# Optimization experiments

Hardware: AMD Instinct MI355X
Metric: run time of the kernel (lower is better)

Reference implementation:

```python
import jax, jax.numpy as jnp
import numpy as np

DIM = 8      # channels (from CxWxW_Attention(8, 4, False))
HEADS = 4    # num_heads
EPS = 1e-12  # torch F.normalize eps


def setup_inputs() -> dict:
    key = jax.random.key(0)
    k0, k1, k2, k3 = jax.random.split(key, 4)
    b, c, h, w = 16, DIM, 512, 512
    x = jax.random.normal(k0, (b, c, h, w), jnp.float32)
    # 1x1 conv producing qkv (bias=False): weight (3c, c)
    w_qkv = jax.random.normal(k1, (3 * c, c), jnp.float32) * 0.1
    # 3x3 depthwise conv on qkv, groups=3c: weight (3c, 1, 3, 3)
    w_dw = jax.random.normal(k2, (3 * c, 1, 3, 3), jnp.float32) * 0.1
    # 1x1 projection out: weight (c, c)
    w_out = jax.random.normal(k3, (c, c), jnp.float32) * 0.1
    # per-head learned temperature, init ones; broadcasts over (b, head, c, w, w)
    temperature = jnp.ones((HEADS, 1, 1, 1), jnp.float32)
    return dict(x=x, w_qkv=w_qkv, w_dw=w_dw, w_out=w_out, temperature=temperature)


def _dwconv3x3(x, wgt):
    # depthwise 3x3, padding=1, groups = channels
    C = x.shape[1]
    return jax.lax.conv_general_dilated(
        x, wgt, window_strides=(1, 1), padding=((1, 1), (1, 1)),
        dimension_numbers=("NCHW", "OIHW", "NCHW"), feature_group_count=C)


def _l2norm(t):
    # torch.nn.functional.normalize along last dim
    n = jnp.sqrt(jnp.sum(t * t, axis=-1, keepdims=True))
    return t / jnp.maximum(n, EPS)


def reference(x, w_qkv, w_dw, w_out, temperature):
    b, c, h, w = x.shape
    heads, ch = HEADS, c // HEADS
    # qkv = dwconv3x3(conv1x1(x))
    qkv = jnp.einsum("bchw,oc->bohw", x, w_qkv)
    qkv = _dwconv3x3(qkv, w_dw)
    q, k, v = jnp.split(qkv, 3, axis=1)
    # rearrange 'b (head ch) h w -> b head ch w h' : width attends, height = feature
    def split_heads(t):
        return t.reshape(b, heads, ch, h, w).transpose(0, 1, 2, 4, 3)
    q, k, v = split_heads(q), split_heads(k), split_heads(v)
    q = _l2norm(q)
    k = _l2norm(k)
    # attention map of shape (b, head, ch, W, W)  -> the 'C x W x W' attention
    attn = jnp.einsum("bncwh,bncvh->bncwv", q, k) * temperature
    attn = jax.nn.softmax(attn, axis=-1)
    out = jnp.einsum("bncwv,bncvh->bncwh", attn, v)  # (b, head, ch, w, h)
    # rearrange back 'b head ch w h -> b (head ch) h w'
    out = out.transpose(0, 1, 2, 4, 3).reshape(b, c, h, w)
    return jnp.einsum("bchw,oc->bohw", out, w_out)
```

## Files before the change

### kernel.cpp

```cpp
#include <hip/hip_runtime.h>
#include <hip/hip_bf16.h>

typedef __attribute__((ext_vector_type(4))) float f32x4;
typedef __attribute__((ext_vector_type(2))) float f32x2;
typedef __attribute__((ext_vector_type(8))) short s16x8;
typedef __attribute__((ext_vector_type(4))) short s16x4;
typedef __attribute__((ext_vector_type(4))) unsigned short u16x4;

#define HW 512
#define NSLICE 128

__global__ __launch_bounds__(256) void qkv_fused(
    const float* __restrict__ x, const float* __restrict__ wqkv,
    const float* __restrict__ wdw,
    __hip_bfloat16* __restrict__ qT, __hip_bfloat16* __restrict__ kT,
    __hip_bfloat16* __restrict__ vS,
    float* __restrict__ qss, float* __restrict__ kss)
{
  const int b = blockIdx.y;
  const int tile = blockIdx.x;
  const int h0 = (tile >> 4) * 32;
  const int w0 = (tile & 15) * 32;
  const int tid = threadIdx.x;

  __shared__ float ts[4][1156][2];
  __shared__ __hip_bfloat16 ot[8][32][36];
  __shared__ float colsq[4][8][32];
  __shared__ float wq_s[24][8];
  __shared__ float wd_s[24][12];

  if (tid < 192) wq_s[tid >> 3][tid & 7] = wqkv[tid];
  if (tid < 216) wd_s[tid / 9][tid % 9] = wdw[tid];

  float xr[5][8];
  #pragma unroll
  for (int p = 0; p < 5; ++p) {
    int i = tid + p * 256;
    if (i < 1156) {
      int ih = h0 - 1 + i / 34, iw = w0 - 1 + i % 34;
      bool ok = (ih >= 0 && ih < HW && iw >= 0 && iw < HW);
      #pragma unroll
      for (int c = 0; c < 8; ++c) {
        xr[p][c] = ok ? x[((size_t)(b * 8 + c) * HW + ih) * HW + iw] : 0.f;
      }
    }
  }
  __syncthreads();

  const int tw = tid & 31;
  const int th = tid >> 5;
  const int lane = tid & 63;
  const int wv = tid >> 6;

  #pragma unroll
  for (int g = 0; g < 3; ++g) {
    #pragma unroll
    for (int p = 0; p < 5; ++p) {
      int i = tid + p * 256;
      if (i < 1156) {
        #pragma unroll
        for (int op = 0; op < 4; ++op) {
          const int o = g * 8 + op * 2;
          float a0 = 0.f, a1 = 0.f;
          #pragma unroll
          for (int c = 0; c < 8; ++c) {
            a0 += xr[p][c] * wq_s[o][c];
            a1 += xr[p][c] * wq_s[o + 1][c];
          }
          ts[op][i][0] = a0;
          ts[op][i][1] = a1;
        }
      }
    }
    __syncthreads();

    #pragma unroll
    for (int op = 0; op < 4; ++op) {
      const int o = g * 8 + op * 2;
      float w2[6][3][2];
      #pragma unroll
      for (int r = 0; r < 6; ++r)
        #pragma unroll
        for (int c = 0; c < 3; ++c) {
          f32x2 v = *(const f32x2*)&ts[op][(4 * th + r) * 34 + tw + c][0];
          w2[r][c][0] = v[0];
          w2[r][c][1] = v[1];
        }
      float o0[4], o1[4];
      #pragma unroll
      for (int r = 0; r < 4; ++r) { o0[r] = 0.f; o1[r] = 0.f; }
      #pragma unroll
      for (int di = 0; di < 3; ++di)
        #pragma unroll
        for (int dj = 0; dj < 3; ++dj) {
          const float wd0 = wd_s[o][di * 3 + dj];
          const float wd1 = wd_s[o + 1][di * 3 + dj];
          #pragma unroll
          for (int r = 0; r < 4; ++r) {
            o0[r] += w2[r + di][dj][0] * wd0;
            o1[r] += w2[r + di][dj][1] * wd1;
          }
        }
      if (g < 2) {
        float s0 = o0[0] * o0[0] + o0[1] * o0[1] + o0[2] * o0[2] + o0[3] * o0[3];
        float s1 = o1[0] * o1[0] + o1[1] * o1[1] + o1[2] * o1[2] + o1[3] * o1[3];
        s0 += __shfl_xor(s0, 32);
        s1 += __shfl_xor(s1, 32);
        if (lane < 32) {
          colsq[wv][op * 2][tw] = s0;
          colsq[wv][op * 2 + 1][tw] = s1;
        }
        #pragma unroll
        for (int r = 0; r < 4; ++r) {
          ot[op * 2][tw][4 * th + r] = __float2bfloat16(o0[r]);
          ot[op * 2 + 1][tw][4 * th + r] = __float2bfloat16(o1[r]);
        }
      } else {
        #pragma unroll
        for (int r = 0; r < 4; ++r) {
          ot[op * 2][4 * th + r][tw] = __float2bfloat16(o0[r]);
          ot[op * 2 + 1][4 * th + r][tw] = __float2bfloat16(o1[r]);
        }
      }
    }
    __syncthreads();

    {
      const int rr = tid >> 3, cc = tid & 7;
      #pragma unroll
      for (int o = 0; o < 8; ++o) {
        s16x4 v = *(const s16x4*)&ot[o][rr][cc * 4];
        const size_t sb = (size_t)(b * 8 + o) * HW * HW;
        if (g == 0) {
          *(s16x4*)(qT + sb + (size_t)(h0 >> 5) * HW * 32 + (size_t)(w0 + rr) * 32 + cc * 4) = v;
        } else if (g == 1) {
          *(s16x4*)(kT + sb + (size_t)(h0 >> 5) * HW * 32 + (size_t)(w0 + rr) * 32 + cc * 4) = v;
        } else {
          *(s16x4*)(vS + sb + (size_t)(w0 >> 5) * HW * 32 + (size_t)(h0 + rr) * 32 + cc * 4) = v;
        }
      }
    }
    if (g < 2) {
      const int o = tid >> 5, w = tid & 31;
      float s = colsq[0][o][w] + colsq[1][o][w] + colsq[2][o][w] + colsq[3][o][w];
      float* dst = (g == 0 ? qss : kss) + (size_t)(b * 8 + o) * HW + w0 + w;
      atomicAdd(dst, s);
    }
  }
}

#define LDS_P    0
#define OFF_RMAX 65536
#define OFF_RSUM 67584
#define OFF_RMAXF 69632
#define OFF_RSINV 69888
#define OFF_SQ   70144
#define OFF_SK   70400
#define ATTN_LDS_SIZE 72448

#define LOADQ(AF, S) { \
    const size_t cq_ = (size_t)(S) * 32768 + klo; \
    _Pragma("unroll") for (int m_ = 0; m_ < 4; ++m_) \
      AF[m_] = *(const s16x8*)(qs + cq_ + (size_t)(w0 + m_ * 16 + arow) * 64); }
#define LOADK(BF, S) { \
    const size_t ck_ = (size_t)(S) * 32768 + klo; \
    _Pragma("unroll") for (int n_ = 0; n_ < 4; ++n_) \
      BF[n_] = *(const s16x8*)(ks + ck_ + (size_t)(wv * 64 + n_ * 16 + arow) * 64); }
#define LOADV(BF, S) { \
    const size_t cv_ = (size_t)(S) * 32768 + klo; \
    _Pragma("unroll") for (int n_ = 0; n_ < 4; ++n_) \
      BF[n_] = *(const s16x8*)(vs + cv_ + (size_t)(wv * 64 + n_ * 16 + arow) * 64); }
#define LOADP(AF, S) { \
    const int cbp_ = (S) * 64 + klo; \
    _Pragma("unroll") for (int m_ = 0; m_ < 4; ++m_) { \
      const int row_ = m_ * 16 + arow; \
      AF[m_] = *(const s16x8*)(ldsP + row_ * 1024 + (cbp_ ^ ((row_ & 7) << 4))); } }
#define MFMA16(AF, BF, ACC) { \
    _Pragma("unroll") for (int m_ = 0; m_ < 4; ++m_) \
      _Pragma("unroll") for (int n_ = 0; n_ < 4; ++n_) \
        ACC[m_][n_] = __builtin_amdgcn_mfma_f32_16x16x32_bf16(AF[m_], BF[n_], ACC[m_][n_], 0, 0, 0); }

__global__ __launch_bounds__(512, 1) void attn_kernel(
    const __hip_bfloat16* __restrict__ qT, const __hip_bfloat16* __restrict__ kT,
    const __hip_bfloat16* __restrict__ vS, __hip_bfloat16* __restrict__ Obuf,
    const float* __restrict__ qss, const float* __restrict__ kss,
    const float* __restrict__ temp)
{
  extern __shared__ char smem[];
  char* ldsP = smem + LDS_P;
  float* red_max  = (float*)(smem + OFF_RMAX);
  float* red_sum  = (float*)(smem + OFF_RSUM);
  float* red_maxf = (float*)(smem + OFF_RMAXF);
  float* rsinv    = (float*)(smem + OFF_RSINV);
  float* sq_l     = (float*)(smem + OFF_SQ);
  float* sk_l     = (float*)(smem + OFF_SK);

  const int tid = threadIdx.x;
  const int lane = tid & 63;
  const int wv = tid >> 6;
  const int p = blockIdx.x;
  const int slice = (p & 7) + 8 * (p >> 6);
  const int rblk = (p >> 3) & 7;
  const int w0 = rblk * 64;
  const size_t sbase = (size_t)slice * HW * HW;
  const char* qs = (const char*)(qT + sbase);
  const char* ks = (const char*)(kT + sbase);
  const char* vs = (const char*)(vS + sbase);

  const int klo = (lane >> 4) << 4;
  const int arow = lane & 15;

  f32x4 acc[4][4];
  #pragma unroll
  for (int m = 0; m < 4; ++m)
    #pragma unroll
    for (int n = 0; n < 4; ++n) acc[m][n] = (f32x4){0.f, 0.f, 0.f, 0.f};

  const float tmp = temp[(slice & 7) >> 1];
  if (tid < 64) sq_l[tid] = tmp / fmaxf(sqrtf(qss[(size_t)slice * HW + w0 + tid]), 1e-12f);
  sk_l[tid] = 1.f / fmaxf(sqrtf(kss[(size_t)slice * HW + tid]), 1e-12f);

  for (int chn = 0; chn < 16; ++chn) {
    s16x8 af[4], bf[4];
    LOADQ(af, chn)
    LOADK(bf, chn)
    MFMA16(af, bf, acc)
  }
  __syncthreads();

  float srow[4][4], scol[4];
  #pragma unroll
  for (int m = 0; m < 4; ++m)
    #pragma unroll
    for (int r = 0; r < 4; ++r)
      srow[m][r] = sq_l[m * 16 + ((lane >> 4) << 2) + r];
  #pragma unroll
  for (int n = 0; n < 4; ++n) scol[n] = sk_l[wv * 64 + n * 16 + (lane & 15)];

  float rmax[4][4];
  #pragma unroll
  for (int m = 0; m < 4; ++m)
    #pragma unroll
    for (int r = 0; r < 4; ++r) {
      float mx = -1e30f;
      #pragma unroll
      for (int n = 0; n < 4; ++n) {
        float v = acc[m][n][r] * srow[m][r] * scol[n];
        acc[m][n][r] = v;
        mx = fmaxf(mx, v);
      }
      mx = fmaxf(mx, __shfl_xor(mx, 1));
      mx = fmaxf(mx, __shfl_xor(mx, 2));
      mx = fmaxf(mx, __shfl_xor(mx, 4));
      mx = fmaxf(mx, __shfl_xor(mx, 8));
      rmax[m][r] = mx;
    }
  if ((lane & 15) == 0) {
    #pragma unroll
    for (int m = 0; m < 4; ++m)
      #pragma unroll
      for (int r = 0; r < 4; ++r)
        red_max[(m * 16 + ((lane >> 4) << 2) + r) * 8 + wv] = rmax[m][r];
  }
  __syncthreads();
  if (tid < 64) {
    float mx = red_max[tid * 8];
    #pragma unroll
    for (int g = 1; g < 8; ++g) mx = fmaxf(mx, red_max[tid * 8 + g]);
    red_maxf[tid] = mx;
  }
  __syncthreads();

  float gmax[4][4];
  #pragma unroll
  for (int m = 0; m < 4; ++m)
    #pragma unroll
    for (int r = 0; r < 4; ++r)
      gmax[m][r] = red_maxf[m * 16 + ((lane >> 4) << 2) + r];

  float rs[4][4];
  #pragma unroll
  for (int m = 0; m < 4; ++m)
    #pragma unroll
    for (int r = 0; r < 4; ++r) rs[m][r] = 0.f;
  #pragma unroll
  for (int m = 0; m < 4; ++m)
    #pragma unroll
    for (int n = 0; n < 4; ++n)
      #pragma unroll
      for (int r = 0; r < 4; ++r) {
        int row = m * 16 + ((lane >> 4) << 2) + r;
        int col = wv * 64 + n * 16 + (lane & 15);
        float pv = __expf(acc[m][n][r] - gmax[m][r]);
        rs[m][r] += pv;
        *(__hip_bfloat16*)(ldsP + row * 1024 + ((col * 2) ^ ((row & 7) << 4))) =
            __float2bfloat16(pv);
      }
  #pragma unroll
  for (int m = 0; m < 4; ++m)
    #pragma unroll
    for (int r = 0; r < 4; ++r) {
      float s = rs[m][r];
      s += __shfl_xor(s, 1);
      s += __shfl_xor(s, 2);
      s += __shfl_xor(s, 4);
      s += __shfl_xor(s, 8);
      if ((lane & 15) == 0)
        red_sum[(m * 16 + ((lane >> 4) << 2) + r) * 8 + wv] = s;
    }
  __syncthreads();
  if (tid < 64) {
    float s = 0.f;
    #pragma unroll
    for (int g = 0; g < 8; ++g) s += red_sum[tid * 8 + g];
    rsinv[tid] = 1.f / s;
  }

  f32x4 acc2[4][4];
  #pragma unroll
  for (int m = 0; m < 4; ++m)
    #pragma unroll
    for (int n = 0; n < 4; ++n) acc2[m][n] = (f32x4){0.f, 0.f, 0.f, 0.f};

  for (int chn = 0; chn < 16; ++chn) {
    s16x8 af[4], bf[4];
    LOADP(af, chn)
    LOADV(bf, chn)
    MFMA16(af, bf, acc2)
  }
  __syncthreads();

  float rinv[4][4];
  #pragma unroll
  for (int m = 0; m < 4; ++m)
    #pragma unroll
    for (int r = 0; r < 4; ++r)
      rinv[m][r] = rsinv[m * 16 + ((lane >> 4) << 2) + r];

  char* ldsO = ldsP + wv * 8192;
  #pragma unroll
  for (int m = 0; m < 4; ++m)
    #pragma unroll
    for (int n = 0; n < 4; ++n)
      #pragma unroll
      for (int r = 0; r < 4; ++r) {
        int row = m * 16 + ((lane >> 4) << 2) + r;
        int col = n * 16 + (lane & 15);
        *(__hip_bfloat16*)(ldsO + row * 128 + col * 2) =
            __float2bfloat16(acc2[m][n][r] * rinv[m][r]);
      }
  __syncthreads();
  __hip_bfloat16* ob = Obuf + sbase + (size_t)w0 * HW + wv * 64;
  #pragma unroll
  for (int it = 0; it < 8; ++it) {
    int row = it * 8 + (lane >> 3);
    int c = (lane & 7) << 4;
    s16x8 v = *(const s16x8*)(ldsO + row * 128 + c);
    *(s16x8*)((char*)ob + (size_t)row * 1024 + c) = v;
  }
}

__global__ __launch_bounds__(256) void proj_kernel(
    const __hip_bfloat16* __restrict__ Obuf, const float* __restrict__ wout,
    float* __restrict__ out)
{
  const int b = blockIdx.y;
  const int t = blockIdx.x;
  const int h0 = (t >> 5) * 64;
  const int w0 = (t & 31) * 16;
  const int tid = threadIdx.x;
  __shared__ float os[8][16][65];
  __shared__ float wo_s[64];
  if (tid < 64) wo_s[tid] = wout[tid];
  {
    int r = tid >> 4;
    int c4 = (tid & 15) * 4;
    #pragma unroll
    for (int o = 0; o < 8; ++o) {
      const __hip_bfloat16* p = Obuf + ((size_t)(b * 8 + o) * HW + w0 + r) * HW + h0 + c4;
      u16x4 v = *(const u16x4*)p;
      #pragma unroll
      for (int i = 0; i < 4; ++i)
        os[o][r][c4 + i] = __uint_as_float((unsigned)v[i] << 16);
    }
  }
  __syncthreads();
  const int w = tid & 15;
  #pragma unroll
  for (int ih = 0; ih < 4; ++ih) {
    int h = ih * 16 + (tid >> 4);
    float ov[8];
    #pragma unroll
    for (int o = 0; o < 8; ++o) ov[o] = os[o][w][h];
    #pragma unroll
    for (int jo = 0; jo < 8; ++jo) {
      float a = 0.f;
      #pragma unroll
      for (int o = 0; o < 8; ++o) a += ov[o] * wo_s[jo * 8 + o];
      out[((size_t)(b * 8 + jo) * HW + h0 + h) * HW + w0 + w] = a;
    }
  }
}

extern "C" void kernel_launch(void* const* d_in, const int* in_sizes, int n_in,
                              void* d_out, int out_size, void* d_ws, size_t ws_size,
                              hipStream_t stream) {
  (void)in_sizes; (void)n_in; (void)out_size; (void)ws_size;
  const float* x    = (const float*)d_in[0];
  const float* wqkv = (const float*)d_in[1];
  const float* wdw  = (const float*)d_in[2];
  const float* wout = (const float*)d_in[3];
  const float* temp = (const float*)d_in[4];
  float* out = (float*)d_out;

  char* ws = (char*)d_ws;
  const size_t plane = (size_t)NSLICE * HW * HW * 2;
  __hip_bfloat16* qT = (__hip_bfloat16*)(ws);
  __hip_bfloat16* kT = (__hip_bfloat16*)(ws + plane);
  __hip_bfloat16* vS = (__hip_bfloat16*)(ws + 2 * plane);
  __hip_bfloat16* Ob = (__hip_bfloat16*)(ws + 3 * plane);
  float* qss = (float*)(ws + 4 * plane);
  float* kss = (float*)(ws + 4 * plane + (size_t)NSLICE * HW * 4);

  hipMemsetAsync(qss, 0, 2 * (size_t)NSLICE * HW * 4, stream);
  qkv_fused<<<dim3(256, 16), 256, 0, stream>>>(x, wqkv, wdw, qT, kT, vS, qss, kss);
  hipFuncSetAttribute((const void*)attn_kernel,
                      hipFuncAttributeMaxDynamicSharedMemorySize, ATTN_LDS_SIZE);
  attn_kernel<<<dim3(1024), 512, ATTN_LDS_SIZE, stream>>>(qT, kT, vS, Ob, qss, kss, temp);
  proj_kernel<<<dim3(256, 16), 256, 0, stream>>>(Ob, wout, out);
}
```

Before: 373.6 us.

## Software-pipeline QK and PV global loads with inline asm and manual vmcnt waits

Replaces the simple per-chunk load-then-MFMA loops in the attention kernel with a four-deep prefetch pipeline. It uses inline-asm global_load_dwordx4 and explicit s_waitcnt vmcnt counts. V tiles are prefetched before the softmax exponent phase so their latency overlaps with exp and LDS writes. This aims to hide global memory latency behind MFMA work, at the cost of many more live VGPRs and fragile hand-managed wait counts that bypass the compiler's scheduling.

```diff
diff --git a/kernel.cpp b/kernel.cpp
--- a/kernel.cpp
+++ b/kernel.cpp
@@ -158,18 +158,26 @@
 #define OFF_SK   70400
 #define ATTN_LDS_SIZE 72448
 
-#define LOADQ(AF, S) { \
-    const size_t cq_ = (size_t)(S) * 32768 + klo; \
-    _Pragma("unroll") for (int m_ = 0; m_ < 4; ++m_) \
-      AF[m_] = *(const s16x8*)(qs + cq_ + (size_t)(w0 + m_ * 16 + arow) * 64); }
-#define LOADK(BF, S) { \
-    const size_t ck_ = (size_t)(S) * 32768 + klo; \
-    _Pragma("unroll") for (int n_ = 0; n_ < 4; ++n_) \
-      BF[n_] = *(const s16x8*)(ks + ck_ + (size_t)(wv * 64 + n_ * 16 + arow) * 64); }
-#define LOADV(BF, S) { \
-    const size_t cv_ = (size_t)(S) * 32768 + klo; \
-    _Pragma("unroll") for (int n_ = 0; n_ < 4; ++n_) \
-      BF[n_] = *(const s16x8*)(vs + cv_ + (size_t)(wv * 64 + n_ * 16 + arow) * 64); }
+#define GL4(D, VOFF, BASE) \
+  asm volatile("global_load_dwordx4 %0, %1, %2 offset:0"    : "=v"(D[0]) : "v"(VOFF), "s"(BASE)); \
+  asm volatile("global_load_dwordx4 %0, %1, %2 offset:1024" : "=v"(D[1]) : "v"(VOFF), "s"(BASE)); \
+  asm volatile("global_load_dwordx4 %0, %1, %2 offset:2048" : "=v"(D[2]) : "v"(VOFF), "s"(BASE)); \
+  asm volatile("global_load_dwordx4 %0, %1, %2 offset:3072" : "=v"(D[3]) : "v"(VOFF), "s"(BASE));
+
+#define LOADSET1(AF, BF, CHN) { \
+  const char* bq_ = qs + (size_t)(CHN) * 32768; \
+  const char* bk_ = ks + (size_t)(CHN) * 32768; \
+  GL4(AF, voffQ, bq_) \
+  GL4(BF, voffK, bk_) }
+
+#define LOADSETV(VF, CHN) { \
+  const char* bv_ = vs + (size_t)(CHN) * 32768; \
+  GL4(VF, voffK, bv_) }
+
+#define WAITV(N) \
+  asm volatile("s_waitcnt vmcnt(" #N ")"); \
+  __builtin_amdgcn_sched_barrier(0);
+
 #define LOADP(AF, S) { \
     const int cbp_ = (S) * 64 + klo; \
     _Pragma("unroll") for (int m_ = 0; m_ < 4; ++m_) { \
@@ -209,6 +217,8 @@
 
   const int klo = (lane >> 4) << 4;
   const int arow = lane & 15;
+  const int voffQ = (w0 + arow) * 64 + klo;
+  const int voffK = (wv * 64 + arow) * 64 + klo;
 
   f32x4 acc[4][4];
   #pragma unroll
@@ -219,13 +229,25 @@
   const float tmp = temp[(slice & 7) >> 1];
   if (tid < 64) sq_l[tid] = tmp / fmaxf(sqrtf(qss[(size_t)slice * HW + w0 + tid]), 1e-12f);
   sk_l[tid] = 1.f / fmaxf(sqrtf(kss[(size_t)slice * HW + tid]), 1e-12f);
-
-  for (int chn = 0; chn < 16; ++chn) {
-    s16x8 af[4], bf[4];
-    LOADQ(af, chn)
-    LOADK(bf, chn)
-    MFMA16(af, bf, acc)
-  }
+  __builtin_amdgcn_sched_barrier(0);
+
+  s16x8 afA[4], bfA[4], afB[4], bfB[4], afC[4], bfC[4], afD[4], bfD[4];
+  LOADSET1(afA, bfA, 0)
+  LOADSET1(afB, bfB, 1)
+  LOADSET1(afC, bfC, 2)
+  LOADSET1(afD, bfD, 3)
+
+  #pragma unroll
+  for (int g = 0; g < 3; ++g) {
+    WAITV(24) MFMA16(afA, bfA, acc) LOADSET1(afA, bfA, 4 * g + 4)
+    WAITV(24) MFMA16(afB, bfB, acc) LOADSET1(afB, bfB, 4 * g + 5)
+    WAITV(24) MFMA16(afC, bfC, acc) LOADSET1(afC, bfC, 4 * g + 6)
+    WAITV(24) MFMA16(afD, bfD, acc) LOADSET1(afD, bfD, 4 * g + 7)
+  }
+  WAITV(24) MFMA16(afA, bfA, acc)
+  WAITV(16) MFMA16(afB, bfB, acc)
+  WAITV(8)  MFMA16(afC, bfC, acc)
+  WAITV(0)  MFMA16(afD, bfD, acc)
   __syncthreads();
 
   float srow[4][4], scol[4];
@@ -277,6 +299,12 @@
     #pragma unroll
     for (int r = 0; r < 4; ++r)
       gmax[m][r] = red_maxf[m * 16 + ((lane >> 4) << 2) + r];
+
+  s16x8 vfA[4], vfB[4], vfC[4], vfD[4];
+  LOADSETV(vfA, 0)
+  LOADSETV(vfB, 1)
+  LOADSETV(vfC, 2)
+  LOADSETV(vfD, 3)
 
   float rs[4][4];
   #pragma unroll
@@ -322,12 +350,17 @@
     #pragma unroll
     for (int n = 0; n < 4; ++n) acc2[m][n] = (f32x4){0.f, 0.f, 0.f, 0.f};
 
-  for (int chn = 0; chn < 16; ++chn) {
-    s16x8 af[4], bf[4];
-    LOADP(af, chn)
-    LOADV(bf, chn)
-    MFMA16(af, bf, acc2)
-  }
+  #pragma unroll
+  for (int g = 0; g < 3; ++g) {
+    WAITV(12) { s16x8 pf[4]; LOADP(pf, 4 * g + 0) MFMA16(pf, vfA, acc2) } LOADSETV(vfA, 4 * g + 4)
+    WAITV(12) { s16x8 pf[4]; LOADP(pf, 4 * g + 1) MFMA16(pf, vfB, acc2) } LOADSETV(vfB, 4 * g + 5)
+    WAITV(12) { s16x8 pf[4]; LOADP(pf, 4 * g + 2) MFMA16(pf, vfC, acc2) } LOADSETV(vfC, 4 * g + 6)
+    WAITV(12) { s16x8 pf[4]; LOADP(pf, 4 * g + 3) MFMA16(pf, vfD, acc2) } LOADSETV(vfD, 4 * g + 7)
+  }
+  WAITV(12) { s16x8 pf[4]; LOADP(pf, 12) MFMA16(pf, vfA, acc2) }
+  WAITV(8)  { s16x8 pf[4]; LOADP(pf, 13) MFMA16(pf, vfB, acc2) }
+  WAITV(4)  { s16x8 pf[4]; LOADP(pf, 14) MFMA16(pf, vfC, acc2) }
+  WAITV(0)  { s16x8 pf[4]; LOADP(pf, 15) MFMA16(pf, vfD, acc2) }
   __syncthreads();
 
   float rinv[4][4];
```

After: 341.6 us. -8.6%, faster.
